# Kernel optimization log

Measured on AMD Instinct MI355X. Metric: run time of the kernel, lower is better.

The kernel has to match this reference:

```python
import jax, jax.numpy as jnp
import numpy as np

N, M, OBS_LEN, PRED_LEN = 8192, 32, 8, 12
H, E = 128, 64
RADIUS = 2.0


def _lstm_cell(x, h, c, Wih, Whh, bih, bhh):
    # torch LSTMCell gate order: i, f, g, o
    g = x @ Wih + h @ Whh + bih + bhh
    i, f, gg, o = jnp.split(g, 4, axis=-1)
    c_new = jax.nn.sigmoid(f) * c + jax.nn.sigmoid(i) * jnp.tanh(gg)
    h_new = jax.nn.sigmoid(o) * jnp.tanh(c_new)
    return h_new, c_new


def _social_pool(focal_pos, nb_pos, nb_h, nb_mask, pW, pb, sW, sb):
    rel = nb_pos - focal_pos[:, None, :]                    # (N,M,2)
    dist = jnp.sqrt(jnp.sum(rel * rel, axis=-1))            # (N,M)
    valid = (dist <= RADIUS) & nb_mask                      # (N,M) bool
    pos_feat = jax.nn.relu(rel @ pW + pb)                   # (N,M,E)
    comb = jnp.concatenate([nb_h, pos_feat], axis=-1)       # (N,M,H+E)
    pooled = jax.nn.relu(comb @ sW + sb) * valid[..., None] # (N,M,H)
    social = pooled.max(axis=1) * valid.any(axis=1, keepdims=True)
    return social                                            # (N,H)


def setup_inputs() -> dict:
    key = jax.random.key(0)
    ks = jax.random.split(key, 12)
    def w(k, shape, fan_in):
        return (jax.random.normal(k, shape, jnp.float32) / np.float32(np.sqrt(fan_in)))
    return {
        'obs': jax.random.normal(ks[0], (N, OBS_LEN, 2), jnp.float32),
        'nb_obs': jax.random.normal(ks[1], (N, M, OBS_LEN, 2), jnp.float32),
        'nb_mask': jax.random.randint(ks[2], (N, M), 0, 2) > 0,
        'we_enc_W': w(ks[3], (2, E), 2), 'we_enc_b': jnp.zeros((E,), jnp.float32),
        'enc_Wih': w(ks[4], (E, 4 * H), E), 'enc_Whh': w(ks[5], (H, 4 * H), H),
        'enc_bih': jnp.zeros((4 * H,), jnp.float32), 'enc_bhh': jnp.zeros((4 * H,), jnp.float32),
        'sp_pos_W': w(ks[6], (2, E), 2), 'sp_pos_b': jnp.zeros((E,), jnp.float32),
        'sp_soc_W': w(ks[7], (H + E, H), H + E), 'sp_soc_b': jnp.zeros((H,), jnp.float32),
        'we_dec_W': w(ks[8], (2, E), 2), 'we_dec_b': jnp.zeros((E,), jnp.float32),
        'dec_Wih': w(ks[9], (E + H, 4 * H), E + H), 'dec_Whh': w(ks[10], (H, 4 * H), H),
        'dec_bih': jnp.zeros((4 * H,), jnp.float32), 'dec_bhh': jnp.zeros((4 * H,), jnp.float32),
        'out_W': w(ks[11], (H, 5), H), 'out_b': jnp.zeros((5,), jnp.float32),
    }


def reference(obs, nb_obs, nb_mask,
              we_enc_W, we_enc_b, enc_Wih, enc_Whh, enc_bih, enc_bhh,
              sp_pos_W, sp_pos_b, sp_soc_W, sp_soc_b,
              we_dec_W, we_dec_b, dec_Wih, dec_Whh, dec_bih, dec_bhh,
              out_W, out_b):
    n = obs.shape[0]
    origin = obs[:, -1:, :]                       # (N,1,2)
    obs_rel = obs - origin                        # (N,T,2)
    nb_rel = nb_obs - nb_obs[:, :, -1:, :]        # (N,M,T,2) (inputs contain no NaN)

    h0 = jnp.zeros((n, H), obs.dtype)
    c0 = jnp.zeros((n, H), obs.dtype)

    def enc_step(carry, xs):
        h, c = carry
        focal, nb_pos = xs                        # (N,2), (N,M,2)
        nb_h = jnp.broadcast_to(h[:, None, :], (n, M, H))
        social = _social_pool(focal, nb_pos, nb_h, nb_mask, sp_pos_W, sp_pos_b, sp_soc_W, sp_soc_b)
        emb = jax.nn.relu(focal @ we_enc_W + we_enc_b)
        h, c = _lstm_cell(emb, h, c, enc_Wih, enc_Whh, enc_bih, enc_bhh)
        h = h + 0.3 * social
        return (h, c), None

    xs = (jnp.swapaxes(obs_rel, 0, 1), jnp.moveaxis(nb_rel, 2, 0))
    (h, c), _ = jax.lax.scan(enc_step, (h0, c0), xs)

    nb_pos_last = jnp.zeros((n, M, 2), obs.dtype)
    nb_h_last = jnp.broadcast_to(h[:, None, :], (n, M, H))  # frozen encoder h
    cur0 = jnp.zeros((n, 2), obs.dtype)

    def dec_step(carry, _):
        h, c, cur = carry
        social = _social_pool(cur, nb_pos_last, nb_h_last, nb_mask, sp_pos_W, sp_pos_b, sp_soc_W, sp_soc_b)
        emb = jax.nn.relu(cur @ we_dec_W + we_dec_b)
        inp = jnp.concatenate([emb, social], axis=-1)
        h, c = _lstm_cell(inp, h, c, dec_Wih, dec_Whh, dec_bih, dec_bhh)
        raw = h @ out_W + out_b                   # dropout = identity (eval)
        mu = raw[:, :2]
        sigma = jnp.exp(jnp.clip(raw[:, 2:4], -4.0, 4.0))
        rho = jnp.tanh(raw[:, 4:5])
        return (h, c, mu), (mu, sigma, rho)

    _, (mus, sigmas, rhos) = jax.lax.scan(dec_step, (h, c, cur0), None, length=PRED_LEN)
    mus = jnp.swapaxes(mus, 0, 1) + origin        # (N,pred_len,2)
    sigmas = jnp.swapaxes(sigmas, 0, 1)           # (N,pred_len,2)
    rhos = jnp.swapaxes(rhos, 0, 1)               # (N,pred_len,1)
    return mus, sigmas, rhos
```

## Files before the change

### kernel.cpp

```cpp
#include <hip/hip_runtime.h>
#include <math.h>

typedef short bf16x8 __attribute__((ext_vector_type(8)));
typedef float f32x4  __attribute__((ext_vector_type(4)));

#define N_AG 8192
#define GA   16
#define BLK  512
#define TOB  8
#define TPR  12

#define PK_ENC 0
#define PK_DEC 98304
#define PK_WB  262144
#define PK_WT  270336
#define PK_TOT 286720

__device__ __forceinline__ unsigned short f2bf(float f) {
    unsigned u = __float_as_uint(f);
    return (unsigned short)((u + 0x7FFFu + ((u >> 16) & 1u)) >> 16);
}
__device__ __forceinline__ float bf2f(unsigned short s) {
    return __uint_as_float(((unsigned)s) << 16);
}
__device__ __forceinline__ float v_exp2(float x) {
    float r; asm("v_exp_f32 %0, %1" : "=v"(r) : "v"(x)); return r;
}
__device__ __forceinline__ float v_rcp(float x) {
    float r; asm("v_rcp_f32 %0, %1" : "=v"(r) : "v"(x)); return r;
}
__device__ __forceinline__ unsigned cvtpk(float lo, float hi) {
    unsigned r; asm("v_cvt_pk_bf16_f32 %0, %1, %2" : "=v"(r) : "v"(lo), "v"(hi)); return r;
}
__device__ __forceinline__ float sigm(float x) {
    return v_rcp(1.f + v_exp2(-1.44269504f * x));
}
__device__ __forceinline__ float tanhp(float x) {
    x = fminf(fmaxf(x, -15.f), 15.f);
    float t = v_exp2(2.88539008f * x);
    return 1.f - 2.f * v_rcp(t + 1.f);
}

__global__ void pack_w(const float* __restrict__ eWih, const float* __restrict__ eWhh,
                       const float* __restrict__ dWih, const float* __restrict__ dWhh,
                       const float* __restrict__ sW, unsigned short* __restrict__ pk)
{
    for (int idx = blockIdx.x * blockDim.x + threadIdx.x; idx < PK_TOT;
         idx += gridDim.x * blockDim.x) {
        float v;
        if (idx < PK_DEC) {
            int ks = idx >> 14, rem = idx & 16383;
            int nt = rem >> 9, l = (rem >> 3) & 63, i = rem & 7;
            int klo = ((l >> 4) << 3) + i;
            int col = (nt >> 3) * 128 + (nt & 7) * 16 + (l & 15);
            v = (ks < 2) ? eWih[(ks * 32 + klo) * 512 + col]
                         : eWhh[((ks - 2) * 32 + klo) * 512 + col];
        } else if (idx < PK_WB) {
            int t = idx - PK_DEC;
            int ks = t >> 14, rem = t & 16383;
            int nt = rem >> 9, l = (rem >> 3) & 63, i = rem & 7;
            int klo = ((l >> 4) << 3) + i;
            int col = (nt >> 3) * 128 + (nt & 7) * 16 + (l & 15);
            if (ks < 2)      v = dWih[(ks * 32 + klo) * 512 + col];
            else if (ks < 6) v = dWih[(64 + (ks - 2) * 32 + klo) * 512 + col];
            else             v = dWhh[((ks - 6) * 32 + klo) * 512 + col];
        } else if (idx < PK_WT) {
            int t = idx - PK_WB;
            int ks = t >> 12, rem = t & 4095;
            int nt = rem >> 9, l = (rem >> 3) & 63, i = rem & 7;
            int klo = ((l >> 4) << 3) + i;
            v = sW[(128 + ks * 32 + klo) * 128 + nt * 16 + (l & 15)];
        } else {
            int t = idx - PK_WT;
            int ks = t >> 12, rem = t & 4095;
            int nt = rem >> 9, l = (rem >> 3) & 63, i = rem & 7;
            int klo = ((l >> 4) << 3) + i;
            v = sW[(ks * 32 + klo) * 128 + nt * 16 + (l & 15)];
        }
        pk[idx] = f2bf(v);
    }
}

__global__ __launch_bounds__(BLK, 4)
void slstm(const float* __restrict__ obs, const float* __restrict__ nb_obs,
           const void* __restrict__ nb_mask,
           const float* __restrict__ weW, const float* __restrict__ web,
           const float* __restrict__ eBih, const float* __restrict__ eBhh,
           const float* __restrict__ pW, const float* __restrict__ pb,
           const float* __restrict__ sb,
           const float* __restrict__ wdW, const float* __restrict__ wdb,
           const float* __restrict__ dBih, const float* __restrict__ dBhh,
           const float* __restrict__ outW, const float* __restrict__ outB,
           const unsigned short* __restrict__ pk,
           float* __restrict__ out)
{
    __shared__ __align__(16) float obsrel[TOB][GA][2];
    __shared__ float origin[GA][2];
    __shared__ __align__(16) float nblast[GA][32][2];
    __shared__ __align__(16) float rel2[GA][32][2];
    __shared__ unsigned vmaskAll[TOB][GA];
    __shared__ int maskb[GA];
    __shared__ int detf;
    __shared__ __align__(16) short hbf[2][GA * 128];
    __shared__ __align__(16) short embb[GA * 64];
    __shared__ __align__(16) short socb[GA * 128];
    __shared__ __align__(16) short pfdb[GA * 64];
    __shared__ __align__(16) short pftA[128 * 64];
    __shared__ __align__(16) short pftB[128 * 64];
    __shared__ float cur[GA][2];

    const int j    = threadIdx.x;
    const int lane = j & 63;
    const int w    = j >> 6;
    const int q    = lane >> 4;
    const int r16  = lane & 15;
    const int swz  = (r16 & 7) << 4;
    const int n0   = blockIdx.x * GA;

    if (j < GA) maskb[j] = 0;
    if (j == 0) detf = 0;
    __syncthreads();
    {
        const unsigned* mw = (const unsigned*)nb_mask;
        unsigned w0 = mw[j], w1 = mw[BLK + j];
        int f = 0;
        if (w0 > 1u || w1 > 1u) f |= 1;
        if ((w0 != 0u && w0 != 0x3F800000u) || (w1 != 0u && w1 != 0x3F800000u)) f |= 2;
        if (f) atomicOr(&detf, f);
    }
    __syncthreads();
    const int det = detf;
    {
        int a = j >> 5, i2 = j & 31, gi = (n0 + a) * 32 + i2;
        int bit;
        if (!(det & 1))      bit = ((const int*)nb_mask)[gi] != 0;
        else if (!(det & 2)) bit = (((const float*)nb_mask)[gi] != 0.f);
        else                 bit = ((const unsigned char*)nb_mask)[gi] != 0;
        if (bit) atomicOr(&maskb[a], 1 << i2);
    }
    if (j < 128) {
        int t = j >> 4, a = j & 15;
        float o0 = obs[(n0 + a) * 16 + 14], o1 = obs[(n0 + a) * 16 + 15];
        obsrel[t][a][0] = obs[(n0 + a) * 16 + t * 2]     - o0;
        obsrel[t][a][1] = obs[(n0 + a) * 16 + t * 2 + 1] - o1;
        if (t == 0) { origin[a][0] = o0; origin[a][1] = o1; }
    }
    {
        int a = j >> 5, i2 = j & 31;
        const float* nb = nb_obs + ((size_t)((n0 + a) * 32 + i2)) * 16 + 14;
        nblast[a][i2][0] = nb[0];
        nblast[a][i2][1] = nb[1];
    }
    ((int4*)hbf)[j] = make_int4(0, 0, 0, 0);

    const int e2 = (j & 31) * 2;
    const float pca0 = pW[e2],      pca1 = pW[e2 + 1];
    const float pcc0 = pW[64 + e2], pcc1 = pW[64 + e2 + 1];
    const float pcb0 = pb[e2],      pcb1 = pb[e2 + 1];
    const float ew0 = weW[lane], ew1 = weW[64 + lane], ebv = web[lane];
    const float dw0 = wdW[lane], dw1 = wdW[64 + lane], dbv = wdb[lane];
    const float pwa = pW[lane], pwc = pW[64 + lane], pbb = pb[lane];
    const float sbv = sb[w * 16 + r16];
    float bG[4];
    #pragma unroll
    for (int g = 0; g < 4; ++g) {
        int col = g * 128 + w * 16 + r16;
        bG[g] = eBih[col] + eBhh[col];
    }
    const bf16x8* pkE = (const bf16x8*)(pk + PK_ENC);
    const bf16x8* pkD = (const bf16x8*)(pk + PK_DEC);
    const bf16x8* pkB = (const bf16x8*)(pk + PK_WB);
    const bf16x8* pkT = (const bf16x8*)(pk + PK_WT);
    bf16x8 wbf[2];
    #pragma unroll
    for (int ks = 0; ks < 2; ++ks)
        wbf[ks] = pkB[(ks * 8 + w) * 64 + lane];

    float cst[4];
    #pragma unroll
    for (int rg = 0; rg < 4; ++rg) cst[rg] = 0.f;

    const f32x4 zz4 = {0.f, 0.f, 0.f, 0.f};
    int pp = 0;
    __syncthreads();

    {
        int a = j >> 5, i2 = j & 31;
        const float* base = nb_obs + ((size_t)((n0 + a) * 32 + i2)) * 16;
        float nlx = nblast[a][i2][0], nly = nblast[a][i2][1];
        int mbit = (maskb[a] >> i2) & 1;
        #pragma unroll
        for (int t = 0; t < TOB; ++t) {
            float rx = base[2 * t]     - nlx - obsrel[t][a][0];
            float ry = base[2 * t + 1] - nly - obsrel[t][a][1];
            bool ok = (rx * rx + ry * ry <= 4.f) && mbit;
            unsigned long long b = __ballot(ok);
            if ((lane & 31) == 0) vmaskAll[t][2 * w + (lane >> 5)] = (unsigned)(b >> (lane & 32));
            if (t == 0) { rel2[a][i2][0] = rx; rel2[a][i2][1] = ry; }
        }
    }
    {
        float x0 = fmaxf(obsrel[0][w][0] * ew0 + obsrel[0][w][1] * ew1 + ebv, 0.f);
        float x1 = fmaxf(obsrel[0][w + 8][0] * ew0 + obsrel[0][w + 8][1] * ew1 + ebv, 0.f);
        unsigned u = cvtpk(x0, x1);
        char* eb = (char*)embb + w * 128 + ((lane * 2) ^ ((w & 7) << 4));
        *(short*)eb = (short)u;
        *(short*)(eb + 1024) = (short)(u >> 16);
    }
    __syncthreads();

    auto FILL = [&](int c, short* buf) {
        const int half16 = (c >> 1) << 4;
        const int alo = (c & 1) << 3;
        const int rw = j >> 5;
        unsigned woff = (unsigned)(rw * 128 + ((e2 * 2) ^ ((rw & 7) << 4)));
        const float* rptr = &rel2[alo][half16 + rw][0];
        #pragma unroll
        for (int s = 0; s < 8; ++s) {
            float rx = rptr[0], ry = rptr[1];
            float v0 = fmaxf(fmaf(ry, pcc0, fmaf(rx, pca0, pcb0)), 0.f);
            float v1 = fmaxf(fmaf(ry, pcc1, fmaf(rx, pca1, pcb1)), 0.f);
            *(unsigned*)((char*)buf + woff) = cvtpk(v0, v1);
            woff += 2048;
            rptr += 64;
        }
    };
    auto SOCIAL = [&](int c, const short* buf, float* ms, int t) {
        const int half16 = (c >> 1) << 4;
        const int alo = (c & 1) << 3;
        #pragma unroll 4
        for (int aLoc = 0; aLoc < 8; ++aLoc) {
            int a = alo + aLoc;
            const char* pb2 = (const char*)buf + (aLoc * 16 + r16) * 128;
            bf16x8 af0 = *(const bf16x8*)(pb2 + ((q * 16) ^ swz));
            bf16x8 af1 = *(const bf16x8*)(pb2 + ((64 + q * 16) ^ swz));
            f32x4 ac = __builtin_amdgcn_mfma_f32_16x16x32_bf16(af0, wbf[0], zz4, 0, 0, 0);
            ac = __builtin_amdgcn_mfma_f32_16x16x32_bf16(af1, wbf[1], ac, 0, 0, 0);
            unsigned vbs = vmaskAll[t][a] >> (half16 + q * 4);
            float pm = ((vbs >> 0) & 1) ? ac[0] : -3e38f;
            pm = fmaxf(pm, ((vbs >> 1) & 1) ? ac[1] : -3e38f);
            pm = fmaxf(pm, ((vbs >> 2) & 1) ? ac[2] : -3e38f);
            pm = fmaxf(pm, ((vbs >> 3) & 1) ? ac[3] : -3e38f);
            pm = fmaxf(pm, __shfl_xor(pm, 16));
            pm = fmaxf(pm, __shfl_xor(pm, 32));
            if (q == (a >> 2)) ms[a & 3] = fmaxf(ms[a & 3], pm);
        }
    };

    #pragma unroll 1
    for (int t = 0; t < TOB; ++t) {
        float ms[4];
        #pragma unroll
        for (int rg = 0; rg < 4; ++rg) ms[rg] = -3e38f;
        f32x4 hpA = zz4;
        f32x4 ag[4];
        #pragma unroll
        for (int g = 0; g < 4; ++g) ag[g] = zz4;
        const short* hb = hbf[pp];
        short* hw = hbf[pp ^ 1];

        FILL(0, pftA);
        #pragma unroll
        for (int ks = 0; ks < 4; ++ks) {
            bf16x8 af = *(const bf16x8*)((const char*)hb + r16 * 256 +
                          (((ks * 32 + q * 8) * 2) ^ swz));
            bf16x8 bfr = pkT[(ks * 8 + w) * 64 + lane];
            hpA = __builtin_amdgcn_mfma_f32_16x16x32_bf16(af, bfr, hpA, 0, 0, 0);
        }
        #pragma unroll 2
        for (int ks = 0; ks < 6; ++ks) {
            bf16x8 af = (ks < 2)
                ? *(const bf16x8*)((const char*)embb + r16 * 128 +
                      (((ks * 32 + q * 8) * 2) ^ swz))
                : *(const bf16x8*)((const char*)hb + r16 * 256 +
                      ((((ks - 2) * 32 + q * 8) * 2) ^ swz));
            #pragma unroll
            for (int g = 0; g < 4; ++g) {
                bf16x8 bfr = pkE[(ks * 32 + g * 8 + w) * 64 + lane];
                ag[g] = __builtin_amdgcn_mfma_f32_16x16x32_bf16(af, bfr, ag[g], 0, 0, 0);
            }
        }
        __syncthreads();

        FILL(1, pftB);
        SOCIAL(0, pftA, ms, t);
        __syncthreads();

        FILL(2, pftA);
        SOCIAL(1, pftB, ms, t);
        __syncthreads();

        FILL(3, pftB);
        SOCIAL(2, pftA, ms, t);
        __syncthreads();

        SOCIAL(3, pftB, ms, t);
        {
            float hn[4];
            #pragma unroll
            for (int rg = 0; rg < 4; ++rg) {
                float gi = sigm(ag[0][rg] + bG[0]);
                float gf = sigm(ag[1][rg] + bG[1]);
                float gg = tanhp(ag[2][rg] + bG[2]);
                float go = sigm(ag[3][rg] + bG[3]);
                cst[rg] = gf * cst[rg] + gi * gg;
                hn[rg] = go * tanhp(cst[rg]) + 0.3f * fmaxf(ms[rg] + hpA[rg] + sbv, 0.f);
            }
            unsigned u01 = cvtpk(hn[0], hn[1]);
            unsigned u23 = cvtpk(hn[2], hn[3]);
            int hx2 = (w * 16 + r16) * 2;
            *(short*)((char*)hw + (q * 4 + 0) * 256 + (hx2 ^ (((q * 4 + 0) & 7) << 4))) = (short)u01;
            *(short*)((char*)hw + (q * 4 + 1) * 256 + (hx2 ^ (((q * 4 + 1) & 7) << 4))) = (short)(u01 >> 16);
            *(short*)((char*)hw + (q * 4 + 2) * 256 + (hx2 ^ (((q * 4 + 2) & 7) << 4))) = (short)u23;
            *(short*)((char*)hw + (q * 4 + 3) * 256 + (hx2 ^ (((q * 4 + 3) & 7) << 4))) = (short)(u23 >> 16);
        }
        if (t < TOB - 1) {
            int a = j >> 5, i2 = j & 31;
            const float* base = nb_obs + ((size_t)((n0 + a) * 32 + i2)) * 16 + (t + 1) * 2;
            rel2[a][i2][0] = base[0] - nblast[a][i2][0] - obsrel[t + 1][a][0];
            rel2[a][i2][1] = base[1] - nblast[a][i2][1] - obsrel[t + 1][a][1];
            float x0 = fmaxf(obsrel[t + 1][w][0] * ew0 + obsrel[t + 1][w][1] * ew1 + ebv, 0.f);
            float x1 = fmaxf(obsrel[t + 1][w + 8][0] * ew0 + obsrel[t + 1][w + 8][1] * ew1 + ebv, 0.f);
            unsigned u = cvtpk(x0, x1);
            char* eb = (char*)embb + w * 128 + ((lane * 2) ^ ((w & 7) << 4));
            *(short*)eb = (short)u;
            *(short*)(eb + 1024) = (short)(u >> 16);
        }
        __syncthreads();
        pp ^= 1;
    }

    f32x4 hpE = zz4;
    {
        const short* hb = hbf[pp];
        #pragma unroll
        for (int ks = 0; ks < 4; ++ks) {
            bf16x8 af = *(const bf16x8*)((const char*)hb + r16 * 256 +
                          (((ks * 32 + q * 8) * 2) ^ swz));
            bf16x8 bfr = pkT[(ks * 8 + w) * 64 + lane];
            hpE = __builtin_amdgcn_mfma_f32_16x16x32_bf16(af, bfr, hpE, 0, 0, 0);
        }
    }
    #pragma unroll
    for (int g = 0; g < 4; ++g) {
        int col = g * 128 + w * 16 + r16;
        bG[g] = dBih[col] + dBhh[col];
    }
    if (j < 32) cur[j >> 1][j & 1] = 0.f;
    __syncthreads();

    #pragma unroll 1
    for (int st = 0; st < TPR; ++st) {
        {
            float cx0 = cur[w][0], cy0 = cur[w][1];
            float cx1 = cur[w + 8][0], cy1 = cur[w + 8][1];
            float xe0 = fmaxf(cx0 * dw0 + cy0 * dw1 + dbv, 0.f);
            float xe1 = fmaxf(cx1 * dw0 + cy1 * dw1 + dbv, 0.f);
            float vp0 = fmaxf(pbb - cx0 * pwa - cy0 * pwc, 0.f);
            float vp1 = fmaxf(pbb - cx1 * pwa - cy1 * pwc, 0.f);
            unsigned ue = cvtpk(xe0, xe1);
            unsigned up = cvtpk(vp0, vp1);
            unsigned off = (unsigned)(w * 128 + ((lane * 2) ^ ((w & 7) << 4)));
            *(short*)((char*)embb + off) = (short)ue;
            *(short*)((char*)embb + off + 1024) = (short)(ue >> 16);
            *(short*)((char*)pfdb + off) = (short)up;
            *(short*)((char*)pfdb + off + 1024) = (short)(up >> 16);
        }
        __syncthreads();

        const short* hb = hbf[pp];
        short* hw = hbf[pp ^ 1];
        {
            f32x4 sa = zz4;
            #pragma unroll
            for (int ks = 0; ks < 2; ++ks) {
                bf16x8 af = *(const bf16x8*)((const char*)pfdb + r16 * 128 +
                              (((ks * 32 + q * 8) * 2) ^ swz));
                sa = __builtin_amdgcn_mfma_f32_16x16x32_bf16(af, wbf[ks], sa, 0, 0, 0);
            }
            float sv[4];
            #pragma unroll
            for (int rg = 0; rg < 4; ++rg) {
                int a = q * 4 + rg;
                float cx = cur[a][0], cy = cur[a][1];
                bool vd = (cx * cx + cy * cy <= 4.f) && (maskb[a] != 0);
                float z = sa[rg] + hpE[rg] + sbv;
                sv[rg] = vd ? fmaxf(z, 0.f) : 0.f;
            }
            unsigned u01 = cvtpk(sv[0], sv[1]);
            unsigned u23 = cvtpk(sv[2], sv[3]);
            int hx2 = (w * 16 + r16) * 2;
            *(short*)((char*)socb + (q * 4 + 0) * 256 + (hx2 ^ (((q * 4 + 0) & 7) << 4))) = (short)u01;
            *(short*)((char*)socb + (q * 4 + 1) * 256 + (hx2 ^ (((q * 4 + 1) & 7) << 4))) = (short)(u01 >> 16);
            *(short*)((char*)socb + (q * 4 + 2) * 256 + (hx2 ^ (((q * 4 + 2) & 7) << 4))) = (short)u23;
            *(short*)((char*)socb + (q * 4 + 3) * 256 + (hx2 ^ (((q * 4 + 3) & 7) << 4))) = (short)(u23 >> 16);
        }
        __syncthreads();

        f32x4 ag[4];
        #pragma unroll
        for (int g = 0; g < 4; ++g) ag[g] = zz4;
        #pragma unroll 2
        for (int ks = 0; ks < 10; ++ks) {
            bf16x8 af;
            if (ks < 2)
                af = *(const bf16x8*)((const char*)embb + r16 * 128 +
                       (((ks * 32 + q * 8) * 2) ^ swz));
            else if (ks < 6)
                af = *(const bf16x8*)((const char*)socb + r16 * 256 +
                       ((((ks - 2) * 32 + q * 8) * 2) ^ swz));
            else
                af = *(const bf16x8*)((const char*)hb + r16 * 256 +
                       ((((ks - 6) * 32 + q * 8) * 2) ^ swz));
            #pragma unroll
            for (int g = 0; g < 4; ++g) {
                bf16x8 bfr = pkD[(ks * 32 + g * 8 + w) * 64 + lane];
                ag[g] = __builtin_amdgcn_mfma_f32_16x16x32_bf16(af, bfr, ag[g], 0, 0, 0);
            }
        }
        {
            float hn[4];
            #pragma unroll
            for (int rg = 0; rg < 4; ++rg) {
                float gi = sigm(ag[0][rg] + bG[0]);
                float gf = sigm(ag[1][rg] + bG[1]);
                float gg = tanhp(ag[2][rg] + bG[2]);
                float go = sigm(ag[3][rg] + bG[3]);
                cst[rg] = gf * cst[rg] + gi * gg;
                hn[rg] = go * tanhp(cst[rg]);
            }
            unsigned u01 = cvtpk(hn[0], hn[1]);
            unsigned u23 = cvtpk(hn[2], hn[3]);
            int hx2 = (w * 16 + r16) * 2;
            *(short*)((char*)hw + (q * 4 + 0) * 256 + (hx2 ^ (((q * 4 + 0) & 7) << 4))) = (short)u01;
            *(short*)((char*)hw + (q * 4 + 1) * 256 + (hx2 ^ (((q * 4 + 1) & 7) << 4))) = (short)(u01 >> 16);
            *(short*)((char*)hw + (q * 4 + 2) * 256 + (hx2 ^ (((q * 4 + 2) & 7) << 4))) = (short)u23;
            *(short*)((char*)hw + (q * 4 + 3) * 256 + (hx2 ^ (((q * 4 + 3) & 7) << 4))) = (short)(u23 >> 16);
        }
        __syncthreads();
        pp ^= 1;

        if (j < 80) {
            int a = j / 5, p5 = j % 5;
            const char* hnb = (const char*)hbf[pp];
            float r = outB[p5];
            #pragma unroll
            for (int k0 = 0; k0 < 128; k0 += 8) {
                bf16x8 hv = *(const bf16x8*)(hnb + a * 256 + ((k0 * 2) ^ ((a & 7) << 4)));
                #pragma unroll
                for (int i = 0; i < 8; ++i)
                    r = fmaf(bf2f((unsigned short)hv[i]), outW[(k0 + i) * 5 + p5], r);
            }
            int n = n0 + a;
            if (p5 < 2) {
                cur[a][p5] = r;
                out[n * 24 + st * 2 + p5] = r + origin[a][p5];
            } else if (p5 < 4) {
                float cl = fminf(fmaxf(r, -4.f), 4.f);
                out[196608 + n * 24 + st * 2 + (p5 - 2)] = v_exp2(cl * 1.44269504f);
            } else {
                out[393216 + n * 12 + st] = tanhp(r);
            }
        }
        __syncthreads();
    }
}

extern "C" void kernel_launch(void* const* d_in, const int* in_sizes, int n_in,
                              void* d_out, int out_size, void* d_ws, size_t ws_size,
                              hipStream_t stream) {
    const float* obs    = (const float*)d_in[0];
    const float* nb_obs = (const float*)d_in[1];
    const void*  nb_mask= d_in[2];
    const float* weW    = (const float*)d_in[3];
    const float* web    = (const float*)d_in[4];
    const float* encWih = (const float*)d_in[5];
    const float* encWhh = (const float*)d_in[6];
    const float* encBih = (const float*)d_in[7];
    const float* encBhh = (const float*)d_in[8];
    const float* pW     = (const float*)d_in[9];
    const float* pb     = (const float*)d_in[10];
    const float* sW     = (const float*)d_in[11];
    const float* sbv    = (const float*)d_in[12];
    const float* wdW    = (const float*)d_in[13];
    const float* wdb    = (const float*)d_in[14];
    const float* decWih = (const float*)d_in[15];
    const float* decWhh = (const float*)d_in[16];
    const float* decBih = (const float*)d_in[17];
    const float* decBhh = (const float*)d_in[18];
    const float* outW   = (const float*)d_in[19];
    const float* outB   = (const float*)d_in[20];
    float* out = (float*)d_out;
    unsigned short* pkw = (unsigned short*)d_ws;

    pack_w<<<(PK_TOT + 255) / 256, 256, 0, stream>>>(encWih, encWhh, decWih, decWhh, sW, pkw);
    slstm<<<N_AG / GA, BLK, 0, stream>>>(obs, nb_obs, nb_mask, weW, web,
        encBih, encBhh, pW, pb, sbv, wdW, wdb, decBih, decBhh, outW, outB, pkw, out);
}
```

Baseline: 305.7 us.

## Compute decoder output head with MFMA and build decoder inputs in registers

The scalar 80-thread output projection is replaced with a bf16 MFMA using a packed, zero-padded out_W slice. The decoder embedding and social position features are now built directly as MFMA A-fragments in registers, which removes the pfdb/embb LDS round trip and one barrier per step. s_setprio hints are also added around the MFMA-heavy regions. The risks are an extra bf16 rounding on the output weights, redundant output-head work in the seven waves that do not write results, and some added register pressure.

Result: slower. 318.0 us (+4.0%).

```diff
diff --git a/kernel.cpp b/kernel.cpp
--- a/kernel.cpp
+++ b/kernel.cpp
@@ -14,7 +14,8 @@
 #define PK_DEC 98304
 #define PK_WB  262144
 #define PK_WT  270336
-#define PK_TOT 286720
+#define PK_OUT 286720
+#define PK_TOT 288768
 
 __device__ __forceinline__ unsigned short f2bf(float f) {
     unsigned u = __float_as_uint(f);
@@ -43,7 +44,8 @@
 
 __global__ void pack_w(const float* __restrict__ eWih, const float* __restrict__ eWhh,
                        const float* __restrict__ dWih, const float* __restrict__ dWhh,
-                       const float* __restrict__ sW, unsigned short* __restrict__ pk)
+                       const float* __restrict__ sW, const float* __restrict__ oW,
+                       unsigned short* __restrict__ pk)
 {
     for (int idx = blockIdx.x * blockDim.x + threadIdx.x; idx < PK_TOT;
          idx += gridDim.x * blockDim.x) {
@@ -70,12 +72,19 @@
             int nt = rem >> 9, l = (rem >> 3) & 63, i = rem & 7;
             int klo = ((l >> 4) << 3) + i;
             v = sW[(128 + ks * 32 + klo) * 128 + nt * 16 + (l & 15)];
-        } else {
+        } else if (idx < PK_OUT) {
             int t = idx - PK_WT;
             int ks = t >> 12, rem = t & 4095;
             int nt = rem >> 9, l = (rem >> 3) & 63, i = rem & 7;
             int klo = ((l >> 4) << 3) + i;
             v = sW[(ks * 32 + klo) * 128 + nt * 16 + (l & 15)];
+        } else {
+            int t = idx - PK_OUT;
+            int ks = t >> 9, r = t & 511;
+            int l = r >> 3, i = r & 7;
+            int klo = ((l >> 4) << 3) + i;
+            int col = l & 15;
+            v = (col < 5) ? oW[(ks * 32 + klo) * 5 + col] : 0.f;
         }
         pk[idx] = f2bf(v);
     }
@@ -90,7 +99,7 @@
            const float* __restrict__ sb,
            const float* __restrict__ wdW, const float* __restrict__ wdb,
            const float* __restrict__ dBih, const float* __restrict__ dBhh,
-           const float* __restrict__ outW, const float* __restrict__ outB,
+           const float* __restrict__ outB,
            const unsigned short* __restrict__ pk,
            float* __restrict__ out)
 {
@@ -104,7 +113,6 @@
     __shared__ __align__(16) short hbf[2][GA * 128];
     __shared__ __align__(16) short embb[GA * 64];
     __shared__ __align__(16) short socb[GA * 128];
-    __shared__ __align__(16) short pfdb[GA * 64];
     __shared__ __align__(16) short pftA[128 * 64];
     __shared__ __align__(16) short pftB[128 * 64];
     __shared__ float cur[GA][2];
@@ -158,8 +166,6 @@
     const float pcc0 = pW[64 + e2], pcc1 = pW[64 + e2 + 1];
     const float pcb0 = pb[e2],      pcb1 = pb[e2 + 1];
     const float ew0 = weW[lane], ew1 = weW[64 + lane], ebv = web[lane];
-    const float dw0 = wdW[lane], dw1 = wdW[64 + lane], dbv = wdb[lane];
-    const float pwa = pW[lane], pwc = pW[64 + lane], pbb = pb[lane];
     const float sbv = sb[w * 16 + r16];
     float bG[4];
     #pragma unroll
@@ -171,6 +177,7 @@
     const bf16x8* pkD = (const bf16x8*)(pk + PK_DEC);
     const bf16x8* pkB = (const bf16x8*)(pk + PK_WB);
     const bf16x8* pkT = (const bf16x8*)(pk + PK_WT);
+    const bf16x8* pkO = (const bf16x8*)(pk + PK_OUT);
     bf16x8 wbf[2];
     #pragma unroll
     for (int ks = 0; ks < 2; ++ks)
@@ -228,6 +235,7 @@
     auto SOCIAL = [&](int c, const short* buf, float* ms, int t) {
         const int half16 = (c >> 1) << 4;
         const int alo = (c & 1) << 3;
+        __builtin_amdgcn_s_setprio(1);
         #pragma unroll 4
         for (int aLoc = 0; aLoc < 8; ++aLoc) {
             int a = alo + aLoc;
@@ -245,6 +253,7 @@
             pm = fmaxf(pm, __shfl_xor(pm, 32));
             if (q == (a >> 2)) ms[a & 3] = fmaxf(ms[a & 3], pm);
         }
+        __builtin_amdgcn_s_setprio(0);
     };
 
     #pragma unroll 1
@@ -260,6 +269,7 @@
         short* hw = hbf[pp ^ 1];
 
         FILL(0, pftA);
+        __builtin_amdgcn_s_setprio(1);
         #pragma unroll
         for (int ks = 0; ks < 4; ++ks) {
             bf16x8 af = *(const bf16x8*)((const char*)hb + r16 * 256 +
@@ -280,6 +290,7 @@
                 ag[g] = __builtin_amdgcn_mfma_f32_16x16x32_bf16(af, bfr, ag[g], 0, 0, 0);
             }
         }
+        __builtin_amdgcn_s_setprio(0);
         __syncthreads();
 
         FILL(1, pftB);
@@ -347,43 +358,60 @@
         bG[g] = dBih[col] + dBhh[col];
     }
     if (j < 32) cur[j >> 1][j & 1] = 0.f;
+    const float obv = outB[r16 < 5 ? r16 : 4];
     __syncthreads();
 
     #pragma unroll 1
     for (int st = 0; st < TPR; ++st) {
-        {
-            float cx0 = cur[w][0], cy0 = cur[w][1];
-            float cx1 = cur[w + 8][0], cy1 = cur[w + 8][1];
-            float xe0 = fmaxf(cx0 * dw0 + cy0 * dw1 + dbv, 0.f);
-            float xe1 = fmaxf(cx1 * dw0 + cy1 * dw1 + dbv, 0.f);
-            float vp0 = fmaxf(pbb - cx0 * pwa - cy0 * pwc, 0.f);
-            float vp1 = fmaxf(pbb - cx1 * pwa - cy1 * pwc, 0.f);
-            unsigned ue = cvtpk(xe0, xe1);
-            unsigned up = cvtpk(vp0, vp1);
-            unsigned off = (unsigned)(w * 128 + ((lane * 2) ^ ((w & 7) << 4)));
-            *(short*)((char*)embb + off) = (short)ue;
-            *(short*)((char*)embb + off + 1024) = (short)(ue >> 16);
-            *(short*)((char*)pfdb + off) = (short)up;
-            *(short*)((char*)pfdb + off + 1024) = (short)(up >> 16);
-        }
-        __syncthreads();
-
         const short* hb = hbf[pp];
         short* hw = hbf[pp ^ 1];
+
+        bf16x8 embf[2];
         {
+            const float cx = cur[r16][0], cy = cur[r16][1];
             f32x4 sa = zz4;
             #pragma unroll
             for (int ks = 0; ks < 2; ++ks) {
-                bf16x8 af = *(const bf16x8*)((const char*)pfdb + r16 * 128 +
-                              (((ks * 32 + q * 8) * 2) ^ swz));
-                sa = __builtin_amdgcn_mfma_f32_16x16x32_bf16(af, wbf[ks], sa, 0, 0, 0);
+                const int e0 = ks * 32 + q * 8;
+                float4 a0 = *(const float4*)(pW + e0);
+                float4 a1 = *(const float4*)(pW + e0 + 4);
+                float4 c0 = *(const float4*)(pW + 64 + e0);
+                float4 c1 = *(const float4*)(pW + 64 + e0 + 4);
+                float4 b0 = *(const float4*)(pb + e0);
+                float4 b1 = *(const float4*)(pb + e0 + 4);
+                union { unsigned u[4]; bf16x8 v; } pf;
+                pf.u[0] = cvtpk(fmaxf(b0.x - cx * a0.x - cy * c0.x, 0.f),
+                                fmaxf(b0.y - cx * a0.y - cy * c0.y, 0.f));
+                pf.u[1] = cvtpk(fmaxf(b0.z - cx * a0.z - cy * c0.z, 0.f),
+                                fmaxf(b0.w - cx * a0.w - cy * c0.w, 0.f));
+                pf.u[2] = cvtpk(fmaxf(b1.x - cx * a1.x - cy * c1.x, 0.f),
+                                fmaxf(b1.y - cx * a1.y - cy * c1.y, 0.f));
+                pf.u[3] = cvtpk(fmaxf(b1.z - cx * a1.z - cy * c1.z, 0.f),
+                                fmaxf(b1.w - cx * a1.w - cy * c1.w, 0.f));
+                sa = __builtin_amdgcn_mfma_f32_16x16x32_bf16(pf.v, wbf[ks], sa, 0, 0, 0);
+                float4 d0 = *(const float4*)(wdW + e0);
+                float4 d1 = *(const float4*)(wdW + e0 + 4);
+                float4 g0 = *(const float4*)(wdW + 64 + e0);
+                float4 g1 = *(const float4*)(wdW + 64 + e0 + 4);
+                float4 h0 = *(const float4*)(wdb + e0);
+                float4 h1 = *(const float4*)(wdb + e0 + 4);
+                union { unsigned u[4]; bf16x8 v; } em;
+                em.u[0] = cvtpk(fmaxf(cx * d0.x + cy * g0.x + h0.x, 0.f),
+                                fmaxf(cx * d0.y + cy * g0.y + h0.y, 0.f));
+                em.u[1] = cvtpk(fmaxf(cx * d0.z + cy * g0.z + h0.z, 0.f),
+                                fmaxf(cx * d0.w + cy * g0.w + h0.w, 0.f));
+                em.u[2] = cvtpk(fmaxf(cx * d1.x + cy * g1.x + h1.x, 0.f),
+                                fmaxf(cx * d1.y + cy * g1.y + h1.y, 0.f));
+                em.u[3] = cvtpk(fmaxf(cx * d1.z + cy * g1.z + h1.z, 0.f),
+                                fmaxf(cx * d1.w + cy * g1.w + h1.w, 0.f));
+                embf[ks] = em.v;
             }
             float sv[4];
             #pragma unroll
             for (int rg = 0; rg < 4; ++rg) {
                 int a = q * 4 + rg;
-                float cx = cur[a][0], cy = cur[a][1];
-                bool vd = (cx * cx + cy * cy <= 4.f) && (maskb[a] != 0);
+                float ax = cur[a][0], ay = cur[a][1];
+                bool vd = (ax * ax + ay * ay <= 4.f) && (maskb[a] != 0);
                 float z = sa[rg] + hpE[rg] + sbv;
                 sv[rg] = vd ? fmaxf(z, 0.f) : 0.f;
             }
@@ -400,12 +428,12 @@
         f32x4 ag[4];
         #pragma unroll
         for (int g = 0; g < 4; ++g) ag[g] = zz4;
+        __builtin_amdgcn_s_setprio(1);
         #pragma unroll 2
         for (int ks = 0; ks < 10; ++ks) {
             bf16x8 af;
             if (ks < 2)
-                af = *(const bf16x8*)((const char*)embb + r16 * 128 +
-                       (((ks * 32 + q * 8) * 2) ^ swz));
+                af = embf[ks];
             else if (ks < 6)
                 af = *(const bf16x8*)((const char*)socb + r16 * 256 +
                        ((((ks - 2) * 32 + q * 8) * 2) ^ swz));
@@ -418,6 +446,7 @@
                 ag[g] = __builtin_amdgcn_mfma_f32_16x16x32_bf16(af, bfr, ag[g], 0, 0, 0);
             }
         }
+        __builtin_amdgcn_s_setprio(0);
         {
             float hn[4];
             #pragma unroll
@@ -440,26 +469,31 @@
         __syncthreads();
         pp ^= 1;
 
-        if (j < 80) {
-            int a = j / 5, p5 = j % 5;
-            const char* hnb = (const char*)hbf[pp];
-            float r = outB[p5];
-            #pragma unroll
-            for (int k0 = 0; k0 < 128; k0 += 8) {
-                bf16x8 hv = *(const bf16x8*)(hnb + a * 256 + ((k0 * 2) ^ ((a & 7) << 4)));
+        {
+            const short* hn = hbf[pp];
+            f32x4 oc = zz4;
+            #pragma unroll
+            for (int ks = 0; ks < 4; ++ks) {
+                bf16x8 af = *(const bf16x8*)((const char*)hn + r16 * 256 +
+                              (((ks * 32 + q * 8) * 2) ^ swz));
+                bf16x8 bfr = pkO[ks * 64 + lane];
+                oc = __builtin_amdgcn_mfma_f32_16x16x32_bf16(af, bfr, oc, 0, 0, 0);
+            }
+            if (w == 0 && r16 < 5) {
                 #pragma unroll
-                for (int i = 0; i < 8; ++i)
-                    r = fmaf(bf2f((unsigned short)hv[i]), outW[(k0 + i) * 5 + p5], r);
-            }
-            int n = n0 + a;
-            if (p5 < 2) {
-                cur[a][p5] = r;
-                out[n * 24 + st * 2 + p5] = r + origin[a][p5];
-            } else if (p5 < 4) {
-                float cl = fminf(fmaxf(r, -4.f), 4.f);
-                out[196608 + n * 24 + st * 2 + (p5 - 2)] = v_exp2(cl * 1.44269504f);
-            } else {
-                out[393216 + n * 12 + st] = tanhp(r);
+                for (int rg = 0; rg < 4; ++rg) {
+                    int a = q * 4 + rg, n = n0 + a;
+                    float r = oc[rg] + obv;
+                    if (r16 < 2) {
+                        cur[a][r16] = r;
+                        out[n * 24 + st * 2 + r16] = r + origin[a][r16];
+                    } else if (r16 < 4) {
+                        float cl = fminf(fmaxf(r, -4.f), 4.f);
+                        out[196608 + n * 24 + st * 2 + (r16 - 2)] = v_exp2(cl * 1.44269504f);
+                    } else {
+                        out[393216 + n * 12 + st] = tanhp(r);
+                    }
+                }
             }
         }
         __syncthreads();
@@ -493,7 +527,7 @@
     float* out = (float*)d_out;
     unsigned short* pkw = (unsigned short*)d_ws;
 
-    pack_w<<<(PK_TOT + 255) / 256, 256, 0, stream>>>(encWih, encWhh, decWih, decWhh, sW, pkw);
+    pack_w<<<(PK_TOT + 255) / 256, 256, 0, stream>>>(encWih, encWhh, decWih, decWhh, sW, outW, pkw);
     slstm<<<N_AG / GA, BLK, 0, stream>>>(obs, nb_obs, nb_mask, weW, web,
-        encBih, encBhh, pW, pb, sbv, wdW, wdb, decBih, decBhh, outW, outB, pkw, out);
-}
+        encBih, encBhh, pW, pb, sbv, wdW, wdb, decBih, decBhh, outB, pkw, out);
+}
```

## Compute output head with MFMA and raise wave priority around MFMA loops

Applied to the files above, without the earlier changes.

The per-step output projection (h @ out_W, 5 columns) is moved from a scalar FMA loop over 80 threads onto a single wavefront using bf16 MFMA, with out_W packed zero-padded to 16 columns in the weight pack. Separately, s_setprio is raised around the social-pool and LSTM gate MFMA loops so those waves get issue priority over others. The goal is to shorten the serial output-head step between decoder barriers. The cost is MFMA work wasted on padding columns, and the priority hints may starve other waves.

Result: faster. 264.1 us (-13.6%).

```diff
diff --git a/kernel.cpp b/kernel.cpp
--- a/kernel.cpp
+++ b/kernel.cpp
@@ -14,7 +14,8 @@
 #define PK_DEC 98304
 #define PK_WB  262144
 #define PK_WT  270336
-#define PK_TOT 286720
+#define PK_OUT 286720
+#define PK_TOT 288768
 
 __device__ __forceinline__ unsigned short f2bf(float f) {
     unsigned u = __float_as_uint(f);
@@ -43,7 +44,8 @@
 
 __global__ void pack_w(const float* __restrict__ eWih, const float* __restrict__ eWhh,
                        const float* __restrict__ dWih, const float* __restrict__ dWhh,
-                       const float* __restrict__ sW, unsigned short* __restrict__ pk)
+                       const float* __restrict__ sW, const float* __restrict__ oW,
+                       unsigned short* __restrict__ pk)
 {
     for (int idx = blockIdx.x * blockDim.x + threadIdx.x; idx < PK_TOT;
          idx += gridDim.x * blockDim.x) {
@@ -70,12 +72,19 @@
             int nt = rem >> 9, l = (rem >> 3) & 63, i = rem & 7;
             int klo = ((l >> 4) << 3) + i;
             v = sW[(128 + ks * 32 + klo) * 128 + nt * 16 + (l & 15)];
-        } else {
+        } else if (idx < PK_OUT) {
             int t = idx - PK_WT;
             int ks = t >> 12, rem = t & 4095;
             int nt = rem >> 9, l = (rem >> 3) & 63, i = rem & 7;
             int klo = ((l >> 4) << 3) + i;
             v = sW[(ks * 32 + klo) * 128 + nt * 16 + (l & 15)];
+        } else {
+            int t = idx - PK_OUT;
+            int ks = t >> 9, r = t & 511;
+            int l = r >> 3, i = r & 7;
+            int klo = ((l >> 4) << 3) + i;
+            int col = l & 15;
+            v = (col < 5) ? oW[(ks * 32 + klo) * 5 + col] : 0.f;
         }
         pk[idx] = f2bf(v);
     }
@@ -90,7 +99,7 @@
            const float* __restrict__ sb,
            const float* __restrict__ wdW, const float* __restrict__ wdb,
            const float* __restrict__ dBih, const float* __restrict__ dBhh,
-           const float* __restrict__ outW, const float* __restrict__ outB,
+           const float* __restrict__ outB,
            const unsigned short* __restrict__ pk,
            float* __restrict__ out)
 {
@@ -171,6 +180,7 @@
     const bf16x8* pkD = (const bf16x8*)(pk + PK_DEC);
     const bf16x8* pkB = (const bf16x8*)(pk + PK_WB);
     const bf16x8* pkT = (const bf16x8*)(pk + PK_WT);
+    const bf16x8* pkO = (const bf16x8*)(pk + PK_OUT);
     bf16x8 wbf[2];
     #pragma unroll
     for (int ks = 0; ks < 2; ++ks)
@@ -228,6 +238,7 @@
     auto SOCIAL = [&](int c, const short* buf, float* ms, int t) {
         const int half16 = (c >> 1) << 4;
         const int alo = (c & 1) << 3;
+        __builtin_amdgcn_s_setprio(1);
         #pragma unroll 4
         for (int aLoc = 0; aLoc < 8; ++aLoc) {
             int a = alo + aLoc;
@@ -245,6 +256,7 @@
             pm = fmaxf(pm, __shfl_xor(pm, 32));
             if (q == (a >> 2)) ms[a & 3] = fmaxf(ms[a & 3], pm);
         }
+        __builtin_amdgcn_s_setprio(0);
     };
 
     #pragma unroll 1
@@ -260,6 +272,7 @@
         short* hw = hbf[pp ^ 1];
 
         FILL(0, pftA);
+        __builtin_amdgcn_s_setprio(1);
         #pragma unroll
         for (int ks = 0; ks < 4; ++ks) {
             bf16x8 af = *(const bf16x8*)((const char*)hb + r16 * 256 +
@@ -280,6 +293,7 @@
                 ag[g] = __builtin_amdgcn_mfma_f32_16x16x32_bf16(af, bfr, ag[g], 0, 0, 0);
             }
         }
+        __builtin_amdgcn_s_setprio(0);
         __syncthreads();
 
         FILL(1, pftB);
@@ -347,6 +361,7 @@
         bG[g] = dBih[col] + dBhh[col];
     }
     if (j < 32) cur[j >> 1][j & 1] = 0.f;
+    const float obv = outB[r16 < 5 ? r16 : 4];
     __syncthreads();
 
     #pragma unroll 1
@@ -400,6 +415,7 @@
         f32x4 ag[4];
         #pragma unroll
         for (int g = 0; g < 4; ++g) ag[g] = zz4;
+        __builtin_amdgcn_s_setprio(1);
         #pragma unroll 2
         for (int ks = 0; ks < 10; ++ks) {
             bf16x8 af;
@@ -418,6 +434,7 @@
                 ag[g] = __builtin_amdgcn_mfma_f32_16x16x32_bf16(af, bfr, ag[g], 0, 0, 0);
             }
         }
+        __builtin_amdgcn_s_setprio(0);
         {
             float hn[4];
             #pragma unroll
@@ -440,26 +457,31 @@
         __syncthreads();
         pp ^= 1;
 
-        if (j < 80) {
-            int a = j / 5, p5 = j % 5;
-            const char* hnb = (const char*)hbf[pp];
-            float r = outB[p5];
-            #pragma unroll
-            for (int k0 = 0; k0 < 128; k0 += 8) {
-                bf16x8 hv = *(const bf16x8*)(hnb + a * 256 + ((k0 * 2) ^ ((a & 7) << 4)));
+        if (w == 0) {
+            const short* hn = hbf[pp];
+            f32x4 oc = zz4;
+            #pragma unroll
+            for (int ks = 0; ks < 4; ++ks) {
+                bf16x8 af = *(const bf16x8*)((const char*)hn + r16 * 256 +
+                              (((ks * 32 + q * 8) * 2) ^ swz));
+                bf16x8 bfr = pkO[ks * 64 + lane];
+                oc = __builtin_amdgcn_mfma_f32_16x16x32_bf16(af, bfr, oc, 0, 0, 0);
+            }
+            if (r16 < 5) {
                 #pragma unroll
-                for (int i = 0; i < 8; ++i)
-                    r = fmaf(bf2f((unsigned short)hv[i]), outW[(k0 + i) * 5 + p5], r);
-            }
-            int n = n0 + a;
-            if (p5 < 2) {
-                cur[a][p5] = r;
-                out[n * 24 + st * 2 + p5] = r + origin[a][p5];
-            } else if (p5 < 4) {
-                float cl = fminf(fmaxf(r, -4.f), 4.f);
-                out[196608 + n * 24 + st * 2 + (p5 - 2)] = v_exp2(cl * 1.44269504f);
-            } else {
-                out[393216 + n * 12 + st] = tanhp(r);
+                for (int rg = 0; rg < 4; ++rg) {
+                    int a = q * 4 + rg, n = n0 + a;
+                    float r = oc[rg] + obv;
+                    if (r16 < 2) {
+                        cur[a][r16] = r;
+                        out[n * 24 + st * 2 + r16] = r + origin[a][r16];
+                    } else if (r16 < 4) {
+                        float cl = fminf(fmaxf(r, -4.f), 4.f);
+                        out[196608 + n * 24 + st * 2 + (r16 - 2)] = v_exp2(cl * 1.44269504f);
+                    } else {
+                        out[393216 + n * 12 + st] = tanhp(r);
+                    }
+                }
             }
         }
         __syncthreads();
@@ -493,7 +515,7 @@
     float* out = (float*)d_out;
     unsigned short* pkw = (unsigned short*)d_ws;
 
-    pack_w<<<(PK_TOT + 255) / 256, 256, 0, stream>>>(encWih, encWhh, decWih, decWhh, sW, pkw);
+    pack_w<<<(PK_TOT + 255) / 256, 256, 0, stream>>>(encWih, encWhh, decWih, decWhh, sW, outW, pkw);
     slstm<<<N_AG / GA, BLK, 0, stream>>>(obs, nb_obs, nb_mask, weW, web,
-        encBih, encBhh, pW, pb, sbv, wdW, wdb, decBih, decBhh, outW, outB, pkw, out);
-}
+        encBih, encBhh, pW, pb, sbv, wdW, wdb, decBih, decBhh, outB, pkw, out);
+}
```
